# Optimization experiments

Measured on AMD Instinct MI355X. Metric: run time of the kernel, lower is better.

The kernel has to match this reference:

```python
import jax, jax.numpy as jnp
import numpy as np

T, H, I = 4096, 4096, 11008  # tokens, hidden, intermediate


def setup_inputs() -> dict:
    key = jax.random.key(0)
    k = jax.random.split(key, 6)
    # int8-range quantized activations and weights (stored as int32 for jax matmul)
    x_q = jax.random.randint(k[0], (T, H), -127, 128).astype(jnp.int32)
    w_gate_up = jax.random.randint(k[1], (2 * I, H), -127, 128).astype(jnp.int32)
    w_down = jax.random.randint(k[2], (H, I), -127, 128).astype(jnp.int32)
    # per-token dynamic input scale, per-output-channel weight scales
    x_scale = jax.random.uniform(k[3], (T,), jnp.float32, 1e-4, 2e-2)
    s_w_gate_up = jax.random.uniform(k[4], (2 * I,), jnp.float32, 1e-4, 2e-2)
    s_w_down = jax.random.uniform(k[5], (H,), jnp.float32, 1e-4, 2e-2)
    return {"x_q": x_q, "x_scale": x_scale, "w_gate_up": w_gate_up,
            "s_w_gate_up": s_w_gate_up, "w_down": w_down, "s_w_down": s_w_down}


def reference(x_q, x_scale, w_gate_up, s_w_gate_up, w_down, s_w_down):
    # --- gate_up_proj: W8A8 int8 GEMM + dequant (per-token x per-channel scales) ---
    gu_i32 = jnp.matmul(x_q, w_gate_up.T)                                   # [T, 2I] int32 accum
    gu = gu_i32.astype(jnp.float32) * x_scale[:, None] * s_w_gate_up[None, :]
    gate, up = gu[:, :I], gu[:, I:]
    # --- SiluAndMulQuant: fused SiLU(gate)*up + per-token dynamic requant to int8 ---
    y = jax.nn.silu(gate) * up                                              # [T, I] fp
    s2 = jnp.maximum(jnp.max(jnp.abs(y), axis=-1), 1e-8) / 127.0            # [T] new dynamic scale
    y_q = jnp.clip(jnp.round(y / s2[:, None]), -128.0, 127.0).astype(jnp.int32)
    # --- down_proj: W8A8 int8 GEMM + dequant ---
    out_i32 = jnp.matmul(y_q, w_down.T)                                     # [T, H] int32 accum
    out = out_i32.astype(jnp.float32) * s2[:, None] * s_w_down[None, :]
    return out
```

## Files before the change

kernel.cpp:

```cpp
#include <hip/hip_runtime.h>
#include <cstdint>
#include <cstddef>

#define T_DIM 4096
#define H_DIM 4096
#define I_DIM 11008

typedef int v4i __attribute__((ext_vector_type(4)));

__device__ __forceinline__ void async_copy16(const void* g, void* l) {
  __builtin_amdgcn_global_load_lds(
      (const __attribute__((address_space(1))) void*)g,
      (__attribute__((address_space(3))) void*)l, 16, 0, 0);
}

__device__ __forceinline__ void stage_tile(const int8_t* src, size_t ld,
                                           char* ldsbase, int wave, int lane) {
#pragma unroll
  for (int q = 0; q < 2; ++q) {
    int seg = q * 4 + wave;
    int r = seg * 16 + (lane >> 2);
    int p = lane & 3;
    int c = p ^ ((r >> 1) & 3);
    const int8_t* g = src + (size_t)r * ld + (size_t)c * 16;
    char* lp = ldsbase + seg * 1024;
    async_copy16((const void*)g, (void*)lp);
  }
}

__device__ __forceinline__ v4i frag_load(const char* ldsbase, int rowbase, int lane) {
  int r = rowbase + (lane & 15);
  int c = (lane >> 4) ^ ((r >> 1) & 3);
  return *(const v4i*)(ldsbase + r * 64 + c * 16);
}

__global__ void pack_i8(const int4* __restrict__ src, char4* __restrict__ dst, int n4) {
  int stride = gridDim.x * blockDim.x;
  for (int i = blockIdx.x * blockDim.x + threadIdx.x; i < n4; i += stride) {
    int4 v = src[i];
    char4 c;
    c.x = (char)v.x; c.y = (char)v.y; c.z = (char)v.z; c.w = (char)v.w;
    dst[i] = c;
  }
}

__global__ void zero_u32(unsigned* __restrict__ p, int n) {
  int i = blockIdx.x * blockDim.x + threadIdx.x;
  if (i < n) p[i] = 0u;
}

__global__ __launch_bounds__(256, 2)
void gemm1_silu(const int8_t* __restrict__ x8,
                const int8_t* __restrict__ wgu8,
                const float* __restrict__ x_scale,
                const float* __restrict__ s_wgu,
                float* __restrict__ y,
                unsigned* __restrict__ rowmax) {
  __shared__ __align__(16) char lds[24 * 1024];
  char* ldsA  = lds;
  char* ldsBg = lds + 8192;
  char* ldsBu = lds + 16384;

  const int tid = threadIdx.x;
  const int wave = tid >> 6, lane = tid & 63;
  const int wm = wave >> 1, wn = wave & 1;
  const int m0 = blockIdx.y * 128;
  const int n0 = blockIdx.x * 128;

  v4i accg[4][4], accu[4][4];
  const v4i vzero = {0, 0, 0, 0};
#pragma unroll
  for (int i = 0; i < 4; i++)
#pragma unroll
    for (int j = 0; j < 4; j++) { accg[i][j] = vzero; accu[i][j] = vzero; }

  const int8_t* Ab  = x8 + (size_t)m0 * H_DIM;
  const int8_t* Bgb = wgu8 + (size_t)n0 * H_DIM;
  const int8_t* Bub = wgu8 + ((size_t)I_DIM + (size_t)n0) * H_DIM;

  for (int k0 = 0; k0 < H_DIM; k0 += 64) {
    __syncthreads();
    stage_tile(Ab + k0, H_DIM, ldsA, wave, lane);
    stage_tile(Bgb + k0, H_DIM, ldsBg, wave, lane);
    stage_tile(Bub + k0, H_DIM, ldsBu, wave, lane);
    __syncthreads();

    v4i a[4], bg[4], bu[4];
#pragma unroll
    for (int i = 0; i < 4; i++) a[i]  = frag_load(ldsA,  wm * 64 + i * 16, lane);
#pragma unroll
    for (int j = 0; j < 4; j++) bg[j] = frag_load(ldsBg, wn * 64 + j * 16, lane);
#pragma unroll
    for (int j = 0; j < 4; j++) bu[j] = frag_load(ldsBu, wn * 64 + j * 16, lane);

#pragma unroll
    for (int i = 0; i < 4; i++)
#pragma unroll
      for (int j = 0; j < 4; j++) {
        accg[i][j] = __builtin_amdgcn_mfma_i32_16x16x64_i8(a[i], bg[j], accg[i][j], 0, 0, 0);
        accu[i][j] = __builtin_amdgcn_mfma_i32_16x16x64_i8(a[i], bu[j], accu[i][j], 0, 0, 0);
      }
  }

  const int lr = lane >> 4;
  const int lc = lane & 15;
#pragma unroll
  for (int i = 0; i < 4; i++) {
#pragma unroll
    for (int t = 0; t < 4; t++) {
      const int gr = m0 + wm * 64 + i * 16 + lr * 4 + t;
      const float sx = x_scale[gr];
      float vmax = 0.f;
#pragma unroll
      for (int j = 0; j < 4; j++) {
        const int gc = n0 + wn * 64 + j * 16 + lc;
        float g = (float)accg[i][j][t] * sx * s_wgu[gc];
        float u = (float)accu[i][j][t] * sx * s_wgu[I_DIM + gc];
        float yv = (g / (1.f + expf(-g))) * u;
        y[(size_t)gr * I_DIM + gc] = yv;
        vmax = fmaxf(vmax, fabsf(yv));
      }
#pragma unroll
      for (int off = 1; off < 16; off <<= 1)
        vmax = fmaxf(vmax, __shfl_xor(vmax, off, 64));
      if (lc == 0) atomicMax(&rowmax[gr], __float_as_uint(vmax));
    }
  }
}

__global__ void quantize_y(const float* __restrict__ y,
                           const unsigned* __restrict__ rowmax,
                           int8_t* __restrict__ yq) {
  size_t gid = (size_t)blockIdx.x * blockDim.x + threadIdx.x;
  size_t base = gid * 4;
  if (base >= (size_t)T_DIM * I_DIM) return;
  int row = (int)(base / I_DIM);
  float inv = 127.f / fmaxf(__uint_as_float(rowmax[row]), 1e-8f);
  float4 v = *(const float4*)(y + base);
  char4 q;
  q.x = (char)(int)fminf(127.f, fmaxf(-128.f, rintf(v.x * inv)));
  q.y = (char)(int)fminf(127.f, fmaxf(-128.f, rintf(v.y * inv)));
  q.z = (char)(int)fminf(127.f, fmaxf(-128.f, rintf(v.z * inv)));
  q.w = (char)(int)fminf(127.f, fmaxf(-128.f, rintf(v.w * inv)));
  *(char4*)(yq + base) = q;
}

__global__ __launch_bounds__(256, 2)
void gemm2_scaled(const int8_t* __restrict__ yq8,
                  const int8_t* __restrict__ wd8,
                  const unsigned* __restrict__ rowmax,
                  const float* __restrict__ s_wd,
                  float* __restrict__ out) {
  __shared__ __align__(16) char lds[16 * 1024];
  char* ldsA = lds;
  char* ldsB = lds + 8192;

  const int tid = threadIdx.x;
  const int wave = tid >> 6, lane = tid & 63;
  const int wm = wave >> 1, wn = wave & 1;
  const int m0 = blockIdx.y * 128;
  const int n0 = blockIdx.x * 128;

  v4i acc[4][4];
  const v4i vzero = {0, 0, 0, 0};
#pragma unroll
  for (int i = 0; i < 4; i++)
#pragma unroll
    for (int j = 0; j < 4; j++) acc[i][j] = vzero;

  const int8_t* Ab = yq8 + (size_t)m0 * I_DIM;
  const int8_t* Bb = wd8 + (size_t)n0 * I_DIM;

  for (int k0 = 0; k0 < I_DIM; k0 += 64) {
    __syncthreads();
    stage_tile(Ab + k0, I_DIM, ldsA, wave, lane);
    stage_tile(Bb + k0, I_DIM, ldsB, wave, lane);
    __syncthreads();

    v4i a[4], b[4];
#pragma unroll
    for (int i = 0; i < 4; i++) a[i] = frag_load(ldsA, wm * 64 + i * 16, lane);
#pragma unroll
    for (int j = 0; j < 4; j++) b[j] = frag_load(ldsB, wn * 64 + j * 16, lane);

#pragma unroll
    for (int i = 0; i < 4; i++)
#pragma unroll
      for (int j = 0; j < 4; j++)
        acc[i][j] = __builtin_amdgcn_mfma_i32_16x16x64_i8(a[i], b[j], acc[i][j], 0, 0, 0);
  }

  const int lr = lane >> 4;
  const int lc = lane & 15;
#pragma unroll
  for (int i = 0; i < 4; i++) {
#pragma unroll
    for (int t = 0; t < 4; t++) {
      const int gr = m0 + wm * 64 + i * 16 + lr * 4 + t;
      const float s2 = fmaxf(__uint_as_float(rowmax[gr]), 1e-8f) / 127.f;
#pragma unroll
      for (int j = 0; j < 4; j++) {
        const int gc = n0 + wn * 64 + j * 16 + lc;
        out[(size_t)gr * H_DIM + gc] = (float)acc[i][j][t] * s2 * s_wd[gc];
      }
    }
  }
}

extern "C" void kernel_launch(void* const* d_in, const int* in_sizes, int n_in,
                              void* d_out, int out_size, void* d_ws, size_t ws_size,
                              hipStream_t stream) {
  const int*   x_q     = (const int*)d_in[0];
  const float* x_scale = (const float*)d_in[1];
  const int*   w_gu    = (const int*)d_in[2];
  const float* s_wgu   = (const float*)d_in[3];
  const int*   w_d     = (const int*)d_in[4];
  const float* s_wd    = (const float*)d_in[5];
  float* out = (float*)d_out;

  char* ws = (char*)d_ws;
  const size_t SZ_X8   = (size_t)T_DIM * H_DIM;
  const size_t SZ_WGU8 = (size_t)2 * I_DIM * H_DIM;
  const size_t SZ_WD8  = (size_t)H_DIM * I_DIM;
  const size_t SZ_Y    = (size_t)T_DIM * I_DIM * 4;
  const size_t SZ_YQ   = (size_t)T_DIM * I_DIM;

  int8_t*   x8     = (int8_t*)ws;
  int8_t*   wgu8   = (int8_t*)(ws + SZ_X8);
  int8_t*   wd8    = (int8_t*)(ws + SZ_X8 + SZ_WGU8);
  float*    y      = (float*)(ws + SZ_X8 + SZ_WGU8 + SZ_WD8);
  int8_t*   yq8    = (int8_t*)(ws + SZ_X8 + SZ_WGU8 + SZ_WD8 + SZ_Y);
  unsigned* rowmax = (unsigned*)(ws + SZ_X8 + SZ_WGU8 + SZ_WD8 + SZ_Y + SZ_YQ);

  pack_i8<<<dim3(8192), dim3(256), 0, stream>>>((const int4*)x_q,  (char4*)x8,   (int)(SZ_X8 / 4));
  pack_i8<<<dim3(8192), dim3(256), 0, stream>>>((const int4*)w_gu, (char4*)wgu8, (int)(SZ_WGU8 / 4));
  pack_i8<<<dim3(8192), dim3(256), 0, stream>>>((const int4*)w_d,  (char4*)wd8,  (int)(SZ_WD8 / 4));
  zero_u32<<<dim3(16), dim3(256), 0, stream>>>(rowmax, T_DIM);

  gemm1_silu<<<dim3(I_DIM / 128, T_DIM / 128), dim3(256), 0, stream>>>(
      x8, wgu8, x_scale, s_wgu, y, rowmax);

  quantize_y<<<dim3((unsigned)((size_t)T_DIM * I_DIM / 4 / 256)), dim3(256), 0, stream>>>(
      y, rowmax, yq8);

  gemm2_scaled<<<dim3(H_DIM / 128, T_DIM / 128), dim3(256), 0, stream>>>(
      yq8, wd8, rowmax, s_wd, out);
}
```

Baseline: 1.472 ms.

## Double-buffer LDS, switch to 32x32x32 MFMA, and widen pack/quantize stores

Both GEMMs now double-buffer their LDS tiles: the next K-slice is prefetched asynchronously while the current one is computed, and one barrier per iteration is removed. The MFMA shape changes from 16x16x64 to 32x32x32 with 2x2 per-wave tiles, so each wave issues fewer, larger matrix instructions and does fewer LDS fragment reads. The pack and quantize kernels now write 16 bytes per thread instead of 4. gemm2's launch bounds are raised to 3 blocks per CU. Doubling LDS use may reduce occupancy, especially for gemm1 with 48 KB per block.

```diff
diff --git a/kernel.cpp b/kernel.cpp
--- a/kernel.cpp
+++ b/kernel.cpp
@@ -6,7 +6,8 @@
 #define H_DIM 4096
 #define I_DIM 11008
 
-typedef int v4i __attribute__((ext_vector_type(4)));
+typedef int v4i  __attribute__((ext_vector_type(4)));
+typedef int v16i __attribute__((ext_vector_type(16)));
 
 __device__ __forceinline__ void async_copy16(const void* g, void* l) {
   __builtin_amdgcn_global_load_lds(
@@ -28,19 +29,24 @@
   }
 }
 
-__device__ __forceinline__ v4i frag_load(const char* ldsbase, int rowbase, int lane) {
-  int r = rowbase + (lane & 15);
-  int c = (lane >> 4) ^ ((r >> 1) & 3);
+__device__ __forceinline__ v4i frag32(const char* ldsbase, int rowbase,
+                                      int kc2, int lane) {
+  int r = rowbase + (lane & 31);
+  int c = (kc2 + (lane >> 5)) ^ ((r >> 1) & 3);
   return *(const v4i*)(ldsbase + r * 64 + c * 16);
 }
 
-__global__ void pack_i8(const int4* __restrict__ src, char4* __restrict__ dst, int n4) {
+__global__ void pack_i8(const int4* __restrict__ src, v4i* __restrict__ dst, int n16) {
   int stride = gridDim.x * blockDim.x;
-  for (int i = blockIdx.x * blockDim.x + threadIdx.x; i < n4; i += stride) {
-    int4 v = src[i];
-    char4 c;
-    c.x = (char)v.x; c.y = (char)v.y; c.z = (char)v.z; c.w = (char)v.w;
-    dst[i] = c;
+  for (int i = blockIdx.x * blockDim.x + threadIdx.x; i < n16; i += stride) {
+    int4 a = src[4 * i + 0], b = src[4 * i + 1];
+    int4 c = src[4 * i + 2], d = src[4 * i + 3];
+    v4i o;
+    o[0] = (a.x & 255) | ((a.y & 255) << 8) | ((a.z & 255) << 16) | (a.w << 24);
+    o[1] = (b.x & 255) | ((b.y & 255) << 8) | ((b.z & 255) << 16) | (b.w << 24);
+    o[2] = (c.x & 255) | ((c.y & 255) << 8) | ((c.z & 255) << 16) | (c.w << 24);
+    o[3] = (d.x & 255) | ((d.y & 255) << 8) | ((d.z & 255) << 16) | (d.w << 24);
+    dst[i] = o;
   }
 }
 
@@ -56,10 +62,7 @@
                 const float* __restrict__ s_wgu,
                 float* __restrict__ y,
                 unsigned* __restrict__ rowmax) {
-  __shared__ __align__(16) char lds[24 * 1024];
-  char* ldsA  = lds;
-  char* ldsBg = lds + 8192;
-  char* ldsBu = lds + 16384;
+  __shared__ __align__(16) char lds[49152];
 
   const int tid = threadIdx.x;
   const int wave = tid >> 6, lane = tid & 63;
@@ -67,61 +70,73 @@
   const int m0 = blockIdx.y * 128;
   const int n0 = blockIdx.x * 128;
 
-  v4i accg[4][4], accu[4][4];
-  const v4i vzero = {0, 0, 0, 0};
-#pragma unroll
-  for (int i = 0; i < 4; i++)
-#pragma unroll
-    for (int j = 0; j < 4; j++) { accg[i][j] = vzero; accu[i][j] = vzero; }
+  v16i vzero;
+#pragma unroll
+  for (int e = 0; e < 16; e++) vzero[e] = 0;
+  v16i accg[2][2], accu[2][2];
+#pragma unroll
+  for (int i = 0; i < 2; i++)
+#pragma unroll
+    for (int j = 0; j < 2; j++) { accg[i][j] = vzero; accu[i][j] = vzero; }
 
   const int8_t* Ab  = x8 + (size_t)m0 * H_DIM;
   const int8_t* Bgb = wgu8 + (size_t)n0 * H_DIM;
   const int8_t* Bub = wgu8 + ((size_t)I_DIM + (size_t)n0) * H_DIM;
 
+  stage_tile(Ab, H_DIM, lds, wave, lane);
+  stage_tile(Bgb, H_DIM, lds + 8192, wave, lane);
+  stage_tile(Bub, H_DIM, lds + 16384, wave, lane);
+
+  int cur = 0;
   for (int k0 = 0; k0 < H_DIM; k0 += 64) {
     __syncthreads();
-    stage_tile(Ab + k0, H_DIM, ldsA, wave, lane);
-    stage_tile(Bgb + k0, H_DIM, ldsBg, wave, lane);
-    stage_tile(Bub + k0, H_DIM, ldsBu, wave, lane);
-    __syncthreads();
-
-    v4i a[4], bg[4], bu[4];
-#pragma unroll
-    for (int i = 0; i < 4; i++) a[i]  = frag_load(ldsA,  wm * 64 + i * 16, lane);
-#pragma unroll
-    for (int j = 0; j < 4; j++) bg[j] = frag_load(ldsBg, wn * 64 + j * 16, lane);
-#pragma unroll
-    for (int j = 0; j < 4; j++) bu[j] = frag_load(ldsBu, wn * 64 + j * 16, lane);
-
-#pragma unroll
-    for (int i = 0; i < 4; i++)
-#pragma unroll
-      for (int j = 0; j < 4; j++) {
-        accg[i][j] = __builtin_amdgcn_mfma_i32_16x16x64_i8(a[i], bg[j], accg[i][j], 0, 0, 0);
-        accu[i][j] = __builtin_amdgcn_mfma_i32_16x16x64_i8(a[i], bu[j], accu[i][j], 0, 0, 0);
-      }
-  }
-
-  const int lr = lane >> 4;
-  const int lc = lane & 15;
-#pragma unroll
-  for (int i = 0; i < 4; i++) {
-#pragma unroll
-    for (int t = 0; t < 4; t++) {
-      const int gr = m0 + wm * 64 + i * 16 + lr * 4 + t;
+    char* buf = lds + cur * 24576;
+    if (k0 + 64 < H_DIM) {
+      char* nb = lds + (cur ^ 1) * 24576;
+      stage_tile(Ab + k0 + 64, H_DIM, nb, wave, lane);
+      stage_tile(Bgb + k0 + 64, H_DIM, nb + 8192, wave, lane);
+      stage_tile(Bub + k0 + 64, H_DIM, nb + 16384, wave, lane);
+    }
+#pragma unroll
+    for (int ks = 0; ks < 2; ++ks) {
+      v4i a[2], bg[2], bu[2];
+#pragma unroll
+      for (int i = 0; i < 2; i++) a[i]  = frag32(buf,         wm * 64 + i * 32, ks * 2, lane);
+#pragma unroll
+      for (int j = 0; j < 2; j++) bg[j] = frag32(buf + 8192,  wn * 64 + j * 32, ks * 2, lane);
+#pragma unroll
+      for (int j = 0; j < 2; j++) bu[j] = frag32(buf + 16384, wn * 64 + j * 32, ks * 2, lane);
+#pragma unroll
+      for (int i = 0; i < 2; i++)
+#pragma unroll
+        for (int j = 0; j < 2; j++) {
+          accg[i][j] = __builtin_amdgcn_mfma_i32_32x32x32_i8(a[i], bg[j], accg[i][j], 0, 0, 0);
+          accu[i][j] = __builtin_amdgcn_mfma_i32_32x32x32_i8(a[i], bu[j], accu[i][j], 0, 0, 0);
+        }
+    }
+    cur ^= 1;
+  }
+
+  const int lc = lane & 31;
+  const int lh = lane >> 5;
+#pragma unroll
+  for (int i = 0; i < 2; i++) {
+#pragma unroll
+    for (int r = 0; r < 16; r++) {
+      const int gr = m0 + wm * 64 + i * 32 + (r & 3) + 8 * (r >> 2) + 4 * lh;
       const float sx = x_scale[gr];
       float vmax = 0.f;
 #pragma unroll
-      for (int j = 0; j < 4; j++) {
-        const int gc = n0 + wn * 64 + j * 16 + lc;
-        float g = (float)accg[i][j][t] * sx * s_wgu[gc];
-        float u = (float)accu[i][j][t] * sx * s_wgu[I_DIM + gc];
+      for (int j = 0; j < 2; j++) {
+        const int gc = n0 + wn * 64 + j * 32 + lc;
+        float g = (float)accg[i][j][r] * sx * s_wgu[gc];
+        float u = (float)accu[i][j][r] * sx * s_wgu[I_DIM + gc];
         float yv = (g / (1.f + expf(-g))) * u;
         y[(size_t)gr * I_DIM + gc] = yv;
         vmax = fmaxf(vmax, fabsf(yv));
       }
 #pragma unroll
-      for (int off = 1; off < 16; off <<= 1)
+      for (int off = 1; off < 32; off <<= 1)
         vmax = fmaxf(vmax, __shfl_xor(vmax, off, 64));
       if (lc == 0) atomicMax(&rowmax[gr], __float_as_uint(vmax));
     }
@@ -130,30 +145,33 @@
 
 __global__ void quantize_y(const float* __restrict__ y,
                            const unsigned* __restrict__ rowmax,
-                           int8_t* __restrict__ yq) {
-  size_t gid = (size_t)blockIdx.x * blockDim.x + threadIdx.x;
-  size_t base = gid * 4;
-  if (base >= (size_t)T_DIM * I_DIM) return;
+                           v4i* __restrict__ yq) {
+  size_t i = (size_t)blockIdx.x * blockDim.x + threadIdx.x;
+  if (i >= (size_t)T_DIM * I_DIM / 16) return;
+  size_t base = i * 16;
   int row = (int)(base / I_DIM);
   float inv = 127.f / fmaxf(__uint_as_float(rowmax[row]), 1e-8f);
-  float4 v = *(const float4*)(y + base);
-  char4 q;
-  q.x = (char)(int)fminf(127.f, fmaxf(-128.f, rintf(v.x * inv)));
-  q.y = (char)(int)fminf(127.f, fmaxf(-128.f, rintf(v.y * inv)));
-  q.z = (char)(int)fminf(127.f, fmaxf(-128.f, rintf(v.z * inv)));
-  q.w = (char)(int)fminf(127.f, fmaxf(-128.f, rintf(v.w * inv)));
-  *(char4*)(yq + base) = q;
-}
-
-__global__ __launch_bounds__(256, 2)
+  const float4* p = (const float4*)(y + base);
+  v4i o;
+#pragma unroll
+  for (int q = 0; q < 4; q++) {
+    float4 v = p[q];
+    int b0 = (int)fminf(127.f, fmaxf(-128.f, rintf(v.x * inv)));
+    int b1 = (int)fminf(127.f, fmaxf(-128.f, rintf(v.y * inv)));
+    int b2 = (int)fminf(127.f, fmaxf(-128.f, rintf(v.z * inv)));
+    int b3 = (int)fminf(127.f, fmaxf(-128.f, rintf(v.w * inv)));
+    o[q] = (b0 & 255) | ((b1 & 255) << 8) | ((b2 & 255) << 16) | (b3 << 24);
+  }
+  yq[i] = o;
+}
+
+__global__ __launch_bounds__(256, 3)
 void gemm2_scaled(const int8_t* __restrict__ yq8,
                   const int8_t* __restrict__ wd8,
                   const unsigned* __restrict__ rowmax,
                   const float* __restrict__ s_wd,
                   float* __restrict__ out) {
-  __shared__ __align__(16) char lds[16 * 1024];
-  char* ldsA = lds;
-  char* ldsB = lds + 8192;
+  __shared__ __align__(16) char lds[32768];
 
   const int tid = threadIdx.x;
   const int wave = tid >> 6, lane = tid & 63;
@@ -161,47 +179,58 @@
   const int m0 = blockIdx.y * 128;
   const int n0 = blockIdx.x * 128;
 
-  v4i acc[4][4];
-  const v4i vzero = {0, 0, 0, 0};
-#pragma unroll
-  for (int i = 0; i < 4; i++)
-#pragma unroll
-    for (int j = 0; j < 4; j++) acc[i][j] = vzero;
+  v16i vzero;
+#pragma unroll
+  for (int e = 0; e < 16; e++) vzero[e] = 0;
+  v16i acc[2][2];
+#pragma unroll
+  for (int i = 0; i < 2; i++)
+#pragma unroll
+    for (int j = 0; j < 2; j++) acc[i][j] = vzero;
 
   const int8_t* Ab = yq8 + (size_t)m0 * I_DIM;
   const int8_t* Bb = wd8 + (size_t)n0 * I_DIM;
 
+  stage_tile(Ab, I_DIM, lds, wave, lane);
+  stage_tile(Bb, I_DIM, lds + 8192, wave, lane);
+
+  int cur = 0;
   for (int k0 = 0; k0 < I_DIM; k0 += 64) {
     __syncthreads();
-    stage_tile(Ab + k0, I_DIM, ldsA, wave, lane);
-    stage_tile(Bb + k0, I_DIM, ldsB, wave, lane);
-    __syncthreads();
-
-    v4i a[4], b[4];
-#pragma unroll
-    for (int i = 0; i < 4; i++) a[i] = frag_load(ldsA, wm * 64 + i * 16, lane);
-#pragma unroll
-    for (int j = 0; j < 4; j++) b[j] = frag_load(ldsB, wn * 64 + j * 16, lane);
-
-#pragma unroll
-    for (int i = 0; i < 4; i++)
-#pragma unroll
-      for (int j = 0; j < 4; j++)
-        acc[i][j] = __builtin_amdgcn_mfma_i32_16x16x64_i8(a[i], b[j], acc[i][j], 0, 0, 0);
-  }
-
-  const int lr = lane >> 4;
-  const int lc = lane & 15;
-#pragma unroll
-  for (int i = 0; i < 4; i++) {
-#pragma unroll
-    for (int t = 0; t < 4; t++) {
-      const int gr = m0 + wm * 64 + i * 16 + lr * 4 + t;
+    char* buf = lds + cur * 16384;
+    if (k0 + 64 < I_DIM) {
+      char* nb = lds + (cur ^ 1) * 16384;
+      stage_tile(Ab + k0 + 64, I_DIM, nb, wave, lane);
+      stage_tile(Bb + k0 + 64, I_DIM, nb + 8192, wave, lane);
+    }
+#pragma unroll
+    for (int ks = 0; ks < 2; ++ks) {
+      v4i a[2], b[2];
+#pragma unroll
+      for (int i = 0; i < 2; i++) a[i] = frag32(buf,        wm * 64 + i * 32, ks * 2, lane);
+#pragma unroll
+      for (int j = 0; j < 2; j++) b[j] = frag32(buf + 8192, wn * 64 + j * 32, ks * 2, lane);
+#pragma unroll
+      for (int i = 0; i < 2; i++)
+#pragma unroll
+        for (int j = 0; j < 2; j++)
+          acc[i][j] = __builtin_amdgcn_mfma_i32_32x32x32_i8(a[i], b[j], acc[i][j], 0, 0, 0);
+    }
+    cur ^= 1;
+  }
+
+  const int lc = lane & 31;
+  const int lh = lane >> 5;
+#pragma unroll
+  for (int i = 0; i < 2; i++) {
+#pragma unroll
+    for (int r = 0; r < 16; r++) {
+      const int gr = m0 + wm * 64 + i * 32 + (r & 3) + 8 * (r >> 2) + 4 * lh;
       const float s2 = fmaxf(__uint_as_float(rowmax[gr]), 1e-8f) / 127.f;
 #pragma unroll
-      for (int j = 0; j < 4; j++) {
-        const int gc = n0 + wn * 64 + j * 16 + lc;
-        out[(size_t)gr * H_DIM + gc] = (float)acc[i][j][t] * s2 * s_wd[gc];
+      for (int j = 0; j < 2; j++) {
+        const int gc = n0 + wn * 64 + j * 32 + lc;
+        out[(size_t)gr * H_DIM + gc] = (float)acc[i][j][r] * s2 * s_wd[gc];
       }
     }
   }
@@ -232,16 +261,16 @@
   int8_t*   yq8    = (int8_t*)(ws + SZ_X8 + SZ_WGU8 + SZ_WD8 + SZ_Y);
   unsigned* rowmax = (unsigned*)(ws + SZ_X8 + SZ_WGU8 + SZ_WD8 + SZ_Y + SZ_YQ);
 
-  pack_i8<<<dim3(8192), dim3(256), 0, stream>>>((const int4*)x_q,  (char4*)x8,   (int)(SZ_X8 / 4));
-  pack_i8<<<dim3(8192), dim3(256), 0, stream>>>((const int4*)w_gu, (char4*)wgu8, (int)(SZ_WGU8 / 4));
-  pack_i8<<<dim3(8192), dim3(256), 0, stream>>>((const int4*)w_d,  (char4*)wd8,  (int)(SZ_WD8 / 4));
+  pack_i8<<<dim3(4096), dim3(256), 0, stream>>>((const int4*)x_q,  (v4i*)x8,   (int)(SZ_X8 / 16));
+  pack_i8<<<dim3(4096), dim3(256), 0, stream>>>((const int4*)w_gu, (v4i*)wgu8, (int)(SZ_WGU8 / 16));
+  pack_i8<<<dim3(4096), dim3(256), 0, stream>>>((const int4*)w_d,  (v4i*)wd8,  (int)(SZ_WD8 / 16));
   zero_u32<<<dim3(16), dim3(256), 0, stream>>>(rowmax, T_DIM);
 
   gemm1_silu<<<dim3(I_DIM / 128, T_DIM / 128), dim3(256), 0, stream>>>(
       x8, wgu8, x_scale, s_wgu, y, rowmax);
 
-  quantize_y<<<dim3((unsigned)((size_t)T_DIM * I_DIM / 4 / 256)), dim3(256), 0, stream>>>(
-      y, rowmax, yq8);
+  quantize_y<<<dim3((unsigned)(((size_t)T_DIM * I_DIM / 16 + 255) / 256)), dim3(256), 0, stream>>>(
+      y, rowmax, (v4i*)yq8);
 
   gemm2_scaled<<<dim3(H_DIM / 128, T_DIM / 128), dim3(256), 0, stream>>>(
       yq8, wd8, rowmax, s_wd, out);
```

After: 1.528 ms. +3.8%, slower.
